# Kernel optimization log

Measured on AMD Instinct MI355X. Metric: run time of the kernel, lower is better.

## Reference

```python
import jax, jax.numpy as jnp
import numpy as np
import math

B, F, M, H, W, PD, KS = 2048, 512, 16, 32, 32, 64, 11
K = KS * KS
R = KS // 2
SIGMA = float(KS) / 3.0
HW = H * W


def _pos_encoding(gaze):
    # (B,2) -> (B,PD); interleaved sin/cos per axis
    half = PD // 2
    div = jnp.exp(jnp.arange(0, half, 2, dtype=jnp.float32) * -(math.log(10000.0) / half))  # (half/2,)
    def enc(p):  # p: (B,1)
        s = jnp.sin(p * div)
        c = jnp.cos(p * div)
        return jnp.stack([s, c], axis=-1).reshape(-1, half)
    return jnp.concatenate([enc(gaze[:, 0:1]), enc(gaze[:, 1:2])], axis=1)


def _adaptive_avg_pool3(x):
    # x: (B,C,H,W) -> (B,C,3,3), matching torch AdaptiveAvgPool2d(3)
    def bounds(n):
        return [(int(np.floor(i * n / 3)), int(np.ceil((i + 1) * n / 3))) for i in range(3)]
    hb, wb = bounds(x.shape[2]), bounds(x.shape[3])
    rows = []
    for (h0, h1) in hb:
        cols = [x[:, :, h0:h1, w0:w1].mean(axis=(2, 3)) for (w0, w1) in wb]
        rows.append(jnp.stack(cols, axis=-1))
    return jnp.stack(rows, axis=-2)  # (B,C,3,3)


def _conv(x, k, b):
    y = jax.lax.conv_general_dilated(x, k, (1, 1), 'SAME',
                                     dimension_numbers=('NCHW', 'OIHW', 'NCHW'))
    return y + b[None, :, None, None]


def setup_inputs() -> dict:
    key = jax.random.key(0)
    ks = jax.random.split(key, 20)
    n = lambda i, shp, sc=0.02: (jax.random.normal(ks[i], shp, dtype=jnp.float32) * sc)
    inp = {
        'features': jax.random.normal(ks[0], (B, F), dtype=jnp.float32),
        'cell_state': jax.random.normal(ks[1], (B, M, H, W), dtype=jnp.float32),
        'gaze_coords': jax.random.uniform(ks[2], (B, 2), dtype=jnp.float32),
        # input_gate: Linear(F+PD,256) -> ReLU -> Linear(256,128) -> ReLU
        'w1': n(3, (F + PD, 256)), 'b1': jnp.zeros((256,), jnp.float32),
        'w2': n(4, (256, 128)), 'b2': jnp.zeros((128,), jnp.float32),
        # write_value: Linear(128, M*K)
        'wv': n(5, (128, M * K)), 'bv': jnp.zeros((M * K,), jnp.float32),
        # strength_head: Linear(2M,64) -> ReLU -> Linear(64,1) -> Sigmoid
        'ws1': n(6, (2 * M, 64)), 'bs1': jnp.zeros((64,), jnp.float32),
        'ws2': n(7, (64, 1)), 'bs2': jnp.zeros((1,), jnp.float32),
        # output_gate convs + final linear
        'ck1': n(8, (128, M, 3, 3)), 'cb1': jnp.zeros((128,), jnp.float32),
        'ck2': n(9, (64, 128, 3, 3)), 'cb2': jnp.zeros((64,), jnp.float32),
        'wo': n(10, (64 * 9, 64 * 9)), 'bo': jnp.zeros((64 * 9,), jnp.float32),
    }
    return inp


def reference(features, cell_state, gaze_coords, w1, b1, w2, b2, wv, bv,
              ws1, bs1, ws2, bs2, ck1, cb1, ck2, cb2, wo, bo):
    # --- input gate + write values ---
    pe = _pos_encoding(gaze_coords)
    g = jax.nn.relu(jnp.concatenate([features, pe], axis=1) @ w1 + b1)
    g = jax.nn.relu(g @ w2 + b2)
    write_vals = (g @ wv + bv).reshape(B, K, M)

    # --- neighborhood geometry ---
    offs = jnp.arange(-R, R + 1)
    ox, oy = jnp.meshgrid(offs, offs, indexing='xy')
    ox, oy = ox.reshape(-1), oy.reshape(-1)  # (K,)
    gx = jnp.clip(gaze_coords[:, 0] * (W - 1), 0.0, W - 1.0)
    gy = jnp.clip(gaze_coords[:, 1] * (H - 1), 0.0, H - 1.0)
    x0 = jnp.floor(gx).astype(jnp.int32)
    y0 = jnp.floor(gy).astype(jnp.int32)
    xs = jnp.clip(x0[:, None] + ox[None, :], 0, W - 1)  # (B,K)
    ys = jnp.clip(y0[:, None] + oy[None, :], 0, H - 1)
    dx = xs.astype(jnp.float32) - gx[:, None]
    dy = ys.astype(jnp.float32) - gy[:, None]
    gauss = jnp.exp(-(dx * dx + dy * dy) / max(1e-6, 2.0 * SIGMA ** 2))
    nw = gauss / jnp.maximum(gauss.sum(axis=1, keepdims=True), 1e-8)  # (B,K)

    # --- gather previous values ---
    idx = ys * W + xs  # (B,K) flat indices
    cell_flat = cell_state.reshape(B, M, HW)
    prev = jnp.take_along_axis(cell_flat, idx[:, None, :], axis=2).transpose(0, 2, 1)  # (B,K,M)

    # --- learned per-cell strength gate ---
    gate_in = jnp.concatenate([prev, write_vals], axis=-1)  # (B,K,2M)
    s = jax.nn.relu(gate_in @ ws1 + bs1)
    gstr = jax.nn.sigmoid(s @ ws2 + bs2)  # (B,K,1)
    w_all = nw[:, :, None] * gstr  # (B,K,1)
    new_vals = (1.0 - w_all) * prev + w_all * write_vals  # (B,K,M)

    # --- weighted scatter-add with normalization ---
    b_idx = jnp.arange(B)[:, None]
    den = jnp.zeros((B, HW), jnp.float32).at[b_idx, idx].add(w_all[..., 0])
    num = jnp.zeros((B, HW, M), jnp.float32).at[b_idx, idx].add(w_all * new_vals)
    keep = 1.0 - jnp.minimum(den, 1.0)  # (B,HW)
    updated_flat = keep[:, None, :] * cell_flat + num.transpose(0, 2, 1)
    updated = updated_flat.reshape(B, M, H, W)

    # --- output gate ---
    y = jax.nn.relu(_conv(updated, ck1, cb1))
    y = jax.nn.relu(_conv(y, ck2, cb2))
    y = _adaptive_avg_pool3(y).reshape(B, -1)  # (B,576)
    out = y @ wo + bo
    return out, updated
```

## Files before the change

kernel.cpp:

```cpp
#include <hip/hip_runtime.h>
#include <hip/hip_bf16.h>
#include <math.h>

#define NB 2048
#define NF 512
#define NM 16
#define NK 121
#define NMK 1936

typedef __attribute__((ext_vector_type(8))) short bf16x8;
typedef __attribute__((ext_vector_type(4))) float f32x4;

#define MFMA __builtin_amdgcn_mfma_f32_16x16x32_bf16

static __device__ __forceinline__ unsigned short f2b(float f) {
  unsigned int u = __float_as_uint(f);
  unsigned int lsb = (u >> 16) & 1u;
  u += 0x7fffu + lsb;
  return (unsigned short)(u >> 16);
}

static __device__ __forceinline__ unsigned cvtpk(float lo, float hi) {
  unsigned r;
  asm("v_cvt_pk_bf16_f32 %0, %1, %2" : "=v"(r) : "v"(lo), "v"(hi));
  return r;
}

__global__ __launch_bounds__(256) void k_pack(
    const float* __restrict__ ck1, const float* __restrict__ ck2,
    unsigned short* __restrict__ ap1, unsigned short* __restrict__ ap2) {
  int i = blockIdx.x * 256 + threadIdx.x;
  if (i < 20480) {
    int j = i & 7, lane = (i >> 3) & 63;
    int m2 = (i >> 9) & 1, kc = (i >> 10) % 5, w = i / 5120;
    int c1 = w * 32 + m2 * 16 + (lane & 15);
    int k = kc * 32 + ((lane >> 4) << 3) + j;
    int s = k >> 4, ci = k & 15;
    float v = 0.f;
    if (s < 9) v = ck1[((c1 * 16 + ci) * 3 + s / 3) * 3 + (s % 3)];
    ap1[i] = f2b(v);
  }
  int i2 = i - 20480;
  if (i2 >= 0 && i2 < 73728) {
    int j = i2 & 7, lane = (i2 >> 3) & 63;
    int kc = (i2 >> 9) & 3, s = (i2 >> 11) % 9, mt = i2 / 18432;
    int c2 = mt * 16 + (lane & 15);
    int c1 = kc * 32 + ((lane >> 4) << 3) + j;
    float v = ck2[((c2 * 128 + c1) * 3 + s / 3) * 3 + (s % 3)];
    ap2[i2] = f2b(v);
  }
}

__global__ __launch_bounds__(256) void k_mlp(
    const float* __restrict__ feat, const float* __restrict__ gaze,
    const float* __restrict__ w1, const float* __restrict__ b1,
    const float* __restrict__ w2, const float* __restrict__ b2,
    const float* __restrict__ wv, const float* __restrict__ bv,
    float* __restrict__ wvout) {
  __shared__ float xs[4][576];
  __shared__ float g1[4][256];
  __shared__ float g2[4][128];
  const int t = threadIdx.x;
  const int b0 = blockIdx.x * 4;

  for (int e = t; e < 4 * 512; e += 256) {
    int r = e >> 9, i = e & 511;
    xs[r][i] = feat[(size_t)(b0 + r) * NF + i];
  }
  if (t < 4 * 64) {
    int r = t >> 6, i = t & 63;
    int axis = i >> 5;
    int ii = i & 31;
    int jj = ii >> 1;
    int isc = ii & 1;
    float p = gaze[(size_t)(b0 + r) * 2 + axis];
    float dv = expf(-(float)(2 * jj) * 0.28782313662425575f);
    float ang = p * dv;
    xs[r][512 + i] = isc ? cosf(ang) : sinf(ang);
  }
  __syncthreads();
  {
    float acc[4];
    float bb = b1[t];
#pragma unroll
    for (int r = 0; r < 4; r++) acc[r] = bb;
#pragma unroll 8
    for (int i = 0; i < 576; i++) {
      float w = w1[(size_t)i * 256 + t];
#pragma unroll
      for (int r = 0; r < 4; r++) acc[r] = fmaf(xs[r][i], w, acc[r]);
    }
#pragma unroll
    for (int r = 0; r < 4; r++) g1[r][t] = fmaxf(acc[r], 0.f);
  }
  __syncthreads();
  if (t < 128) {
    float acc[4];
    float bb = b2[t];
#pragma unroll
    for (int r = 0; r < 4; r++) acc[r] = bb;
#pragma unroll 8
    for (int i = 0; i < 256; i++) {
      float w = w2[(size_t)i * 128 + t];
#pragma unroll
      for (int r = 0; r < 4; r++) acc[r] = fmaf(g1[r][i], w, acc[r]);
    }
#pragma unroll
    for (int r = 0; r < 4; r++) g2[r][t] = fmaxf(acc[r], 0.f);
  }
  __syncthreads();
  {
    float acc7[7][4];
    float accT[4];
#pragma unroll
    for (int jj = 0; jj < 7; jj++) {
      float bb = bv[t + 256 * jj];
#pragma unroll
      for (int r = 0; r < 4; r++) acc7[jj][r] = bb;
    }
    {
      float bb = (t < 144) ? bv[1792 + t] : 0.f;
#pragma unroll
      for (int r = 0; r < 4; r++) accT[r] = bb;
    }
#pragma unroll 2
    for (int i = 0; i < 128; i++) {
      float g[4];
#pragma unroll
      for (int r = 0; r < 4; r++) g[r] = g2[r][i];
      const float* wrow = wv + (size_t)i * NMK;
#pragma unroll
      for (int jj = 0; jj < 7; jj++) {
        float w = wrow[t + 256 * jj];
#pragma unroll
        for (int r = 0; r < 4; r++) acc7[jj][r] = fmaf(g[r], w, acc7[jj][r]);
      }
      if (t < 144) {
        float w = wrow[1792 + t];
#pragma unroll
        for (int r = 0; r < 4; r++) accT[r] = fmaf(g[r], w, accT[r]);
      }
    }
#pragma unroll
    for (int r = 0; r < 4; r++) {
      float* orow = wvout + (size_t)(b0 + r) * NMK;
#pragma unroll
      for (int jj = 0; jj < 7; jj++) orow[t + 256 * jj] = acc7[jj][r];
      if (t < 144) orow[1792 + t] = accT[r];
    }
  }
}

__global__ __launch_bounds__(256) void k_update(
    const float* __restrict__ cell, const float* __restrict__ gaze,
    const float* __restrict__ wvin,
    const float* __restrict__ ws1, const float* __restrict__ bs1,
    const float* __restrict__ ws2, const float* __restrict__ bs2,
    float* __restrict__ updated, unsigned short* __restrict__ ubf) {
  __shared__ float numl[16][129];
  __shared__ float denl[128];
  __shared__ float ws1s[2048];
  __shared__ float bs1s[64];
  __shared__ float ws2s[64];
  __shared__ float nws[121];
  __shared__ float z2part[2][128];
  __shared__ float gsum_s;
  __shared__ float bs2s;
  const int t = threadIdx.x;
  const int b = blockIdx.x;
  const int kk = t & 127;
  const int hf = t >> 7;

  for (int e = t; e < 16 * 129; e += 256) ((float*)numl)[e] = 0.f;
  if (t < 128) denl[t] = 0.f;
  for (int e = t; e < 2048; e += 256) ws1s[e] = ws1[e];
  if (t < 64) { bs1s[t] = bs1[t]; ws2s[t] = ws2[t]; }
  if (t == 0) bs2s = bs2[0];

  const float gx = fminf(fmaxf(gaze[(size_t)b * 2 + 0] * 31.f, 0.f), 31.f);
  const float gy = fminf(fmaxf(gaze[(size_t)b * 2 + 1] * 31.f, 0.f), 31.f);
  const int x0 = (int)floorf(gx);
  const int y0 = (int)floorf(gy);
  const int wx0 = max(0, x0 - 5);
  const int wy0 = max(0, y0 - 5);

  int xi = 0, yi = 0;
  if (kk < NK) {
    int ox = kk % 11 - 5;
    int oy = kk / 11 - 5;
    xi = min(max(x0 + ox, 0), 31);
    yi = min(max(y0 + oy, 0), 31);
    if (hf == 0) {
      float dx = (float)xi - gx, dy = (float)yi - gy;
      nws[kk] = expf(-(dx * dx + dy * dy) * (9.0f / 242.0f));
    }
  }
  __syncthreads();
  if (t < 64) {
    float s = nws[t] + ((t + 64 < NK) ? nws[t + 64] : 0.f);
    s += __shfl_xor(s, 1, 64);
    s += __shfl_xor(s, 2, 64);
    s += __shfl_xor(s, 4, 64);
    s += __shfl_xor(s, 8, 64);
    s += __shfl_xor(s, 16, 64);
    s += __shfl_xor(s, 32, 64);
    if (t == 0) gsum_s = fmaxf(s, 1e-8f);
  }
  __syncthreads();

  float prev[16], wvv[16];
  if (kk < NK) {
    const int idx = yi * 32 + xi;
#pragma unroll
    for (int m = 0; m < 16; m++) prev[m] = cell[(size_t)b * 16384 + m * 1024 + idx];
#pragma unroll
    for (int m = 0; m < 16; m++) wvv[m] = wvin[(size_t)b * NMK + kk * 16 + m];
    float z2p = 0.f;
    const int j0 = hf * 32;
    for (int j = j0; j < j0 + 32; j++) {
      float z = bs1s[j];
#pragma unroll
      for (int i = 0; i < 16; i++) z = fmaf(prev[i], ws1s[i * 64 + j], z);
#pragma unroll
      for (int i = 0; i < 16; i++) z = fmaf(wvv[i], ws1s[(16 + i) * 64 + j], z);
      z = fmaxf(z, 0.f);
      z2p = fmaf(z, ws2s[j], z2p);
    }
    z2part[hf][kk] = z2p;
  }
  __syncthreads();

  if (t < NK) {
    const float nw = nws[t] / gsum_s;
    const int local = (yi - wy0) * 11 + (xi - wx0);
    float z2 = bs2s + z2part[0][t] + z2part[1][t];
    float gstr = 1.f / (1.f + expf(-z2));
    float w = nw * gstr;
    atomicAdd(&denl[local], w);
#pragma unroll
    for (int m = 0; m < 16; m++) {
      float nv = (1.f - w) * prev[m] + w * wvv[m];
      atomicAdd(&numl[m][local], w * nv);
    }
  }
  __syncthreads();

  for (int e = t; e < 16384; e += 256) {
    int m = e >> 10, hw = e & 1023;
    int yy = hw >> 5, xx = hw & 31;
    int wy = yy - wy0, wx = xx - wx0;
    float dv = 0.f, nm = 0.f;
    if ((unsigned)wy < 11u && (unsigned)wx < 11u) {
      int local = wy * 11 + wx;
      dv = denl[local];
      nm = numl[m][local];
    }
    float keep = 1.f - fminf(dv, 1.f);
    updated[(size_t)b * 16384 + e] = keep * cell[(size_t)b * 16384 + e] + nm;
  }

  unsigned* ub32 = (unsigned*)ubf + (size_t)b * 9248;
  for (int e = t; e < 8192; e += 256) {
    int p = e & 7;
    int hw = e >> 3;
    int yy = hw >> 5, xx = hw & 31;
    int wy = yy - wy0, wx = xx - wx0;
    float dv = 0.f, n0 = 0.f, n1 = 0.f;
    if ((unsigned)wy < 11u && (unsigned)wx < 11u) {
      int local = wy * 11 + wx;
      dv = denl[local];
      n0 = numl[2 * p][local];
      n1 = numl[2 * p + 1][local];
    }
    float keep = 1.f - fminf(dv, 1.f);
    float v0 = keep * cell[(size_t)b * 16384 + (2 * p) * 1024 + hw] + n0;
    float v1 = keep * cell[(size_t)b * 16384 + (2 * p + 1) * 1024 + hw] + n1;
    ub32[((yy + 1) * 34 + (xx + 1)) * 8 + p] = cvtpk(v0, v1);
  }
  for (int e = t; e < 1056; e += 256) {
    int j = e & 7, pos = e >> 3;
    int row, col;
    if (pos < 34)       { row = 0;             col = pos; }
    else if (pos < 68)  { row = 33;            col = pos - 34; }
    else if (pos < 100) { row = pos - 68 + 1;  col = 0; }
    else                { row = pos - 100 + 1; col = 33; }
    ub32[(row * 34 + col) * 8 + j] = 0u;
  }
}

__global__ __launch_bounds__(256, 2) void k_conv3(
    const unsigned short* __restrict__ ubf,
    const unsigned short* __restrict__ ap1, const float* __restrict__ cb1,
    const unsigned short* __restrict__ ap2, const float* __restrict__ cb2,
    float* __restrict__ ypool) {
  __shared__ unsigned short y1[6][34][136];
  const int t = threadIdx.x;
  const int b = blockIdx.x;
  const int lane = t & 63;
  const int w = t >> 6;
  const int ln = lane & 15;
  const int q = lane >> 4;
  const int qh = q >> 1, ql = q & 1;

  const unsigned short* ubb = ubf + (size_t)b * 18496;

  bf16x8 a2[9][4];
#pragma unroll
  for (int s = 0; s < 9; s++)
#pragma unroll
    for (int kc = 0; kc < 4; kc++)
      a2[s][kc] = *(const bf16x8*)(ap2 + (size_t)((w * 36 + s * 4 + kc) * 64 + lane) * 8);

  f32x4 cb2r;
  {
    int c2b = w * 16 + q * 4;
    cb2r = f32x4{cb2[c2b], cb2[c2b + 1], cb2[c2b + 2], cb2[c2b + 3]};
  }

  int po1[5];
#pragma unroll
  for (int kc = 0; kc < 5; kc++) {
    int s = 2 * kc + qh;
    if (s > 8) s = 0;
    po1[kc] = (s / 3) * 544 + (s % 3) * 16;
  }

  for (int e = t; e < 816; e += 256) {
    int w8 = e % 68;
    int r2 = e / 68;
    ((unsigned*)y1)[(r2 >> 1) * 2312 + ((r2 & 1) ? 2244 : 0) + w8] = 0u;
  }

  f32x4 PL0 = {0.f, 0.f, 0.f, 0.f}, PL1 = PL0, PL2 = PL0;
  f32x4 PH0 = PL0, PH1 = PL0, PH2 = PL0;

#pragma unroll 1
  for (int ti = 0; ti < 8; ti++) {
    const int r0 = ti * 4;

    bf16x8 a1[5][2];
#pragma unroll
    for (int kc = 0; kc < 5; kc++)
#pragma unroll
      for (int m2 = 0; m2 < 2; m2++)
        a1[kc][m2] = *(const bf16x8*)(ap1 + (size_t)(((w * 5 + kc) * 2 + m2) * 64 + lane) * 8);
    f32x4 cb1r[2];
#pragma unroll
    for (int m2 = 0; m2 < 2; m2++) {
      int c1b = w * 32 + m2 * 16 + q * 4;
      cb1r[m2] = f32x4{cb1[c1b], cb1[c1b + 1], cb1[c1b + 2], cb1[c1b + 3]};
    }

#pragma unroll 2
    for (int nt = 0; nt < 12; nt++) {
      const int ry = nt >> 1, h = nt & 1;
      const int gy1 = r0 - 1 + ry;
      const int gyc = min(max(gy1, 0), 31);
      const int x = h * 16 + ln;
      const unsigned short* bp = ubb + gyc * 544 + x * 16 + ql * 8;
      bf16x8 f0 = *(const bf16x8*)(bp + po1[0]);
      bf16x8 f1 = *(const bf16x8*)(bp + po1[1]);
      bf16x8 f2 = *(const bf16x8*)(bp + po1[2]);
      bf16x8 f3 = *(const bf16x8*)(bp + po1[3]);
      bf16x8 f4 = *(const bf16x8*)(bp + po1[4]);
      f32x4 acc0 = cb1r[0], acc1 = cb1r[1];
      acc0 = MFMA(a1[0][0], f0, acc0, 0, 0, 0); acc1 = MFMA(a1[0][1], f0, acc1, 0, 0, 0);
      acc0 = MFMA(a1[1][0], f1, acc0, 0, 0, 0); acc1 = MFMA(a1[1][1], f1, acc1, 0, 0, 0);
      acc0 = MFMA(a1[2][0], f2, acc0, 0, 0, 0); acc1 = MFMA(a1[2][1], f2, acc1, 0, 0, 0);
      acc0 = MFMA(a1[3][0], f3, acc0, 0, 0, 0); acc1 = MFMA(a1[3][1], f3, acc1, 0, 0, 0);
      acc0 = MFMA(a1[4][0], f4, acc0, 0, 0, 0); acc1 = MFMA(a1[4][1], f4, acc1, 0, 0, 0);
      const bool inr = ((unsigned)gy1 < 32u);
#pragma unroll
      for (int m2 = 0; m2 < 2; m2++) {
        f32x4 a = m2 ? acc1 : acc0;
        float v0 = inr ? fmaxf(a[0], 0.f) : 0.f;
        float v1 = inr ? fmaxf(a[1], 0.f) : 0.f;
        float v2 = inr ? fmaxf(a[2], 0.f) : 0.f;
        float v3 = inr ? fmaxf(a[3], 0.f) : 0.f;
        uint2 pk;
        pk.x = cvtpk(v0, v1);
        pk.y = cvtpk(v2, v3);
        *(uint2*)&y1[ry][1 + x][w * 32 + m2 * 16 + q * 4] = pk;
      }
    }
    __syncthreads();

#pragma unroll
    for (int h = 0; h < 2; h++) {
      const int xg = h * 16 + ln;
      const unsigned short* yb = &y1[0][xg][q * 8];
      f32x4 A0 = cb2r, A1 = cb2r, A2 = cb2r, A3 = cb2r;
#pragma unroll
      for (int yr = 0; yr < 6; yr++)
#pragma unroll
        for (int kc = 0; kc < 4; kc++)
#pragma unroll
          for (int dx = 0; dx < 3; dx++) {
            bf16x8 fr = *(const bf16x8*)(yb + yr * 4624 + dx * 136 + kc * 32);
#pragma unroll
            for (int dy = 0; dy < 3; dy++) {
              const int rr = yr - dy;
              if (rr < 0 || rr > 3) continue;
              f32x4& ac = (rr == 0) ? A0 : ((rr == 1) ? A1 : ((rr == 2) ? A2 : A3));
              ac = MFMA(a2[dy * 3 + dx][kc], fr, ac, 0, 0, 0);
            }
          }
#pragma unroll
      for (int rr = 0; rr < 4; rr++) {
        const int grow = r0 + rr;
        const float rm0 = (grow <= 10) ? 1.f : 0.f;
        const float rm1 = (grow >= 10 && grow <= 21) ? 1.f : 0.f;
        const float rm2 = (grow >= 21) ? 1.f : 0.f;
        f32x4 v = (rr == 0) ? A0 : ((rr == 1) ? A1 : ((rr == 2) ? A2 : A3));
        v[0] = fmaxf(v[0], 0.f);
        v[1] = fmaxf(v[1], 0.f);
        v[2] = fmaxf(v[2], 0.f);
        v[3] = fmaxf(v[3], 0.f);
        if (h == 0) {
          PL0 += v * rm0; PL1 += v * rm1; PL2 += v * rm2;
        } else {
          PH0 += v * rm0; PH1 += v * rm1; PH2 += v * rm2;
        }
      }
    }
    __syncthreads();
  }

  const float mA0 = (ln <= 10) ? 1.f : 0.f;
  const float mA1 = (ln >= 10) ? 1.f : 0.f;
  const float mB1 = (ln <= 5) ? 1.f : 0.f;
  const float mB2 = (ln >= 5) ? 1.f : 0.f;
  f32x4 t00 = PL0 * mA0, t01 = PL0 * mA1 + PH0 * mB1, t02 = PH0 * mB2;
  f32x4 t10 = PL1 * mA0, t11 = PL1 * mA1 + PH1 * mB1, t12 = PH1 * mB2;
  f32x4 t20 = PL2 * mA0, t21 = PL2 * mA1 + PH2 * mB1, t22 = PH2 * mB2;

  {
    f32x4* tv[9] = {&t00, &t01, &t02, &t10, &t11, &t12, &t20, &t21, &t22};
#pragma unroll
    for (int i = 0; i < 9; i++) {
      f32x4& v = *tv[i];
#pragma unroll
      for (int c = 0; c < 4; c++) {
        float s = v[c];
        s += __shfl_xor(s, 1, 64);
        s += __shfl_xor(s, 2, 64);
        s += __shfl_xor(s, 4, 64);
        s += __shfl_xor(s, 8, 64);
        v[c] = s;
      }
    }
  }

  float* yp = ypool + (size_t)b * 576 + (w * 16 + q * 4) * 9;
#define PWRITE(tv, ph, pw)                                                      \
  if (ln == (ph * 3 + pw)) {                                                    \
    const float dv = 1.f / (float)(((ph == 1) ? 12 : 11) * ((pw == 1) ? 12 : 11)); \
    yp[0 * 9 + ph * 3 + pw] = tv[0] * dv;                                       \
    yp[1 * 9 + ph * 3 + pw] = tv[1] * dv;                                       \
    yp[2 * 9 + ph * 3 + pw] = tv[2] * dv;                                       \
    yp[3 * 9 + ph * 3 + pw] = tv[3] * dv;                                       \
  }
  PWRITE(t00, 0, 0) PWRITE(t01, 0, 1) PWRITE(t02, 0, 2)
  PWRITE(t10, 1, 0) PWRITE(t11, 1, 1) PWRITE(t12, 1, 2)
  PWRITE(t20, 2, 0) PWRITE(t21, 2, 1) PWRITE(t22, 2, 2)
#undef PWRITE
}

__global__ __launch_bounds__(256) void k_out(
    const float* __restrict__ ypool, const float* __restrict__ wo,
    const float* __restrict__ bo, float* __restrict__ out) {
  __shared__ float ys[8][576];
  const int t = threadIdx.x;
  const int b0 = blockIdx.x * 8;
  for (int e = t; e < 8 * 576; e += 256) {
    int r = e / 576, i = e % 576;
    ys[r][i] = ypool[(size_t)(b0 + r) * 576 + i];
  }
  __syncthreads();
  for (int j = t; j < 576; j += 256) {
    float acc[8];
    float bb = bo[j];
#pragma unroll
    for (int r = 0; r < 8; r++) acc[r] = bb;
#pragma unroll 4
    for (int i = 0; i < 576; i++) {
      float w = wo[(size_t)i * 576 + j];
#pragma unroll
      for (int r = 0; r < 8; r++) acc[r] = fmaf(ys[r][i], w, acc[r]);
    }
#pragma unroll
    for (int r = 0; r < 8; r++) out[(size_t)(b0 + r) * 576 + j] = acc[r];
  }
}

extern "C" void kernel_launch(void* const* d_in, const int* in_sizes, int n_in,
                              void* d_out, int out_size, void* d_ws, size_t ws_size,
                              hipStream_t stream) {
  (void)in_sizes; (void)n_in; (void)out_size;
  const float* feat = (const float*)d_in[0];
  const float* cell = (const float*)d_in[1];
  const float* gaze = (const float*)d_in[2];
  const float* w1   = (const float*)d_in[3];
  const float* b1   = (const float*)d_in[4];
  const float* w2   = (const float*)d_in[5];
  const float* b2   = (const float*)d_in[6];
  const float* wv   = (const float*)d_in[7];
  const float* bv   = (const float*)d_in[8];
  const float* ws1  = (const float*)d_in[9];
  const float* bs1  = (const float*)d_in[10];
  const float* ws2  = (const float*)d_in[11];
  const float* bs2  = (const float*)d_in[12];
  const float* ck1  = (const float*)d_in[13];
  const float* cb1  = (const float*)d_in[14];
  const float* ck2  = (const float*)d_in[15];
  const float* cb2  = (const float*)d_in[16];
  const float* wo   = (const float*)d_in[17];
  const float* bo   = (const float*)d_in[18];

  float* out0    = (float*)d_out;
  float* updated = out0 + (size_t)NB * 576;
  float* wvout   = (float*)d_ws;
  float* ypool   = wvout + (size_t)NB * NMK;
  unsigned short* ap1 = (unsigned short*)(ypool + (size_t)NB * 576);
  unsigned short* ap2 = ap1 + 20480;
  unsigned short* ubf = ap2 + 73728;

  const size_t fixed_bytes = ((size_t)NB * (NMK + 576)) * 4 + (size_t)94208 * 2;
  const size_t wsz = ws_size ? ws_size : ((size_t)1 << 30);
  int chunk = 2048;
  while (chunk > 128 && fixed_bytes + (size_t)chunk * 36992 > wsz) chunk >>= 1;

  k_pack<<<dim3(368), dim3(256), 0, stream>>>(ck1, ck2, ap1, ap2);
  k_mlp<<<dim3(NB / 4), dim3(256), 0, stream>>>(feat, gaze, w1, b1, w2, b2, wv, bv, wvout);
  for (int b0 = 0; b0 < NB; b0 += chunk) {
    const int n = (NB - b0 < chunk) ? (NB - b0) : chunk;
    k_update<<<dim3(n), dim3(256), 0, stream>>>(
        cell + (size_t)b0 * 16384, gaze + (size_t)b0 * 2,
        wvout + (size_t)b0 * NMK, ws1, bs1, ws2, bs2,
        updated + (size_t)b0 * 16384, ubf);
    k_conv3<<<dim3(n), dim3(256), 0, stream>>>(
        ubf, ap1, cb1, ap2, cb2, ypool + (size_t)b0 * 576);
  }
  k_out<<<dim3(NB / 8), dim3(256), 0, stream>>>(ypool, wo, bo, out0);
}
```

Before: 1.093 ms.

## Use ring buffer for conv1 rows, raise occupancy, restructure output GEMV

The conv3 kernel now keeps a 6-slot ring buffer of conv1 output rows, so each tile after the first computes only 4 new rows instead of recomputing 6 including the halo rows. The shared buffer drops the padding column (the right-edge read wraps to a zero column), and launch bounds ask for 3 blocks per SM. The output linear kernel handles 4 batch rows per block with twice as many blocks and fixed per-thread column assignments. The ring buffer relies on the zeroed halo slots and the wrap indexing staying correct, and the higher occupancy target may force register spills given the large a2 register array.

```diff
diff --git a/kernel.cpp b/kernel.cpp
--- a/kernel.cpp
+++ b/kernel.cpp
@@ -288,12 +288,13 @@
   }
 }
 
-__global__ __launch_bounds__(256, 2) void k_conv3(
+#define Y1ROW 4488
+__global__ __launch_bounds__(256, 3) void k_conv3(
     const unsigned short* __restrict__ ubf,
     const unsigned short* __restrict__ ap1, const float* __restrict__ cb1,
     const unsigned short* __restrict__ ap2, const float* __restrict__ cb2,
     float* __restrict__ ypool) {
-  __shared__ unsigned short y1[6][34][136];
+  __shared__ unsigned short y1[6][33][136];
   const int t = threadIdx.x;
   const int b = blockIdx.x;
   const int lane = t & 63;
@@ -325,10 +326,9 @@
     po1[kc] = (s / 3) * 544 + (s % 3) * 16;
   }
 
-  for (int e = t; e < 816; e += 256) {
-    int w8 = e % 68;
-    int r2 = e / 68;
-    ((unsigned*)y1)[(r2 >> 1) * 2312 + ((r2 & 1) ? 2244 : 0) + w8] = 0u;
+  for (int e = t; e < 6 * 68; e += 256) {
+    int s = e / 68, wd = e % 68;
+    ((unsigned*)y1)[s * (Y1ROW / 2) + wd] = 0u;
   }
 
   f32x4 PL0 = {0.f, 0.f, 0.f, 0.f}, PL1 = PL0, PL2 = PL0;
@@ -351,10 +351,13 @@
       cb1r[m2] = f32x4{cb1[c1b], cb1[c1b + 1], cb1[c1b + 2], cb1[c1b + 3]};
     }
 
+    const int nrow = (ti == 0) ? 6 : 4;
+    const int abase = (ti == 0) ? -1 : r0 + 1;
 #pragma unroll 2
-    for (int nt = 0; nt < 12; nt++) {
+    for (int nt = 0; nt < nrow * 2; nt++) {
       const int ry = nt >> 1, h = nt & 1;
-      const int gy1 = r0 - 1 + ry;
+      const int gy1 = abase + ry;
+      const int slot = (gy1 + 1) % 6;
       const int gyc = min(max(gy1, 0), 31);
       const int x = h * 16 + ln;
       const unsigned short* bp = ubb + gyc * 544 + x * 16 + ql * 8;
@@ -380,15 +383,34 @@
         uint2 pk;
         pk.x = cvtpk(v0, v1);
         pk.y = cvtpk(v2, v3);
-        *(uint2*)&y1[ry][1 + x][w * 32 + m2 * 16 + q * 4] = pk;
+        *(uint2*)&y1[slot][1 + x][w * 32 + m2 * 16 + q * 4] = pk;
       }
     }
     __syncthreads();
 
+    int rowoff[6];
+    {
+      int s0 = (r0) % 6;
+#pragma unroll
+      for (int yr = 0; yr < 6; yr++) {
+        int s = s0 + yr;
+        if (s >= 6) s -= 6;
+        rowoff[yr] = s * Y1ROW;
+      }
+    }
 #pragma unroll
     for (int h = 0; h < 2; h++) {
       const int xg = h * 16 + ln;
-      const unsigned short* yb = &y1[0][xg][q * 8];
+      const unsigned short* rp[6];
+#pragma unroll
+      for (int yr = 0; yr < 6; yr++) rp[yr] = &y1[0][0][0] + rowoff[yr] + q * 8;
+      int pco[3];
+#pragma unroll
+      for (int dx = 0; dx < 3; dx++) {
+        int pc = xg + dx;
+        if (pc == 33) pc = 0;
+        pco[dx] = pc * 136;
+      }
       f32x4 A0 = cb2r, A1 = cb2r, A2 = cb2r, A3 = cb2r;
 #pragma unroll
       for (int yr = 0; yr < 6; yr++)
@@ -396,7 +418,7 @@
         for (int kc = 0; kc < 4; kc++)
 #pragma unroll
           for (int dx = 0; dx < 3; dx++) {
-            bf16x8 fr = *(const bf16x8*)(yb + yr * 4624 + dx * 136 + kc * 32);
+            bf16x8 fr = *(const bf16x8*)(rp[yr] + pco[dx] + kc * 32);
 #pragma unroll
             for (int dy = 0; dy < 3; dy++) {
               const int rr = yr - dy;
@@ -469,27 +491,45 @@
 __global__ __launch_bounds__(256) void k_out(
     const float* __restrict__ ypool, const float* __restrict__ wo,
     const float* __restrict__ bo, float* __restrict__ out) {
-  __shared__ float ys[8][576];
+  __shared__ float ys[4][576];
   const int t = threadIdx.x;
-  const int b0 = blockIdx.x * 8;
-  for (int e = t; e < 8 * 576; e += 256) {
+  const int b0 = blockIdx.x * 4;
+  for (int e = t; e < 4 * 576; e += 256) {
     int r = e / 576, i = e % 576;
     ys[r][i] = ypool[(size_t)(b0 + r) * 576 + i];
   }
   __syncthreads();
-  for (int j = t; j < 576; j += 256) {
-    float acc[8];
-    float bb = bo[j];
-#pragma unroll
-    for (int r = 0; r < 8; r++) acc[r] = bb;
-#pragma unroll 4
-    for (int i = 0; i < 576; i++) {
-      float w = wo[(size_t)i * 576 + j];
-#pragma unroll
-      for (int r = 0; r < 8; r++) acc[r] = fmaf(ys[r][i], w, acc[r]);
-    }
-#pragma unroll
-    for (int r = 0; r < 8; r++) out[(size_t)(b0 + r) * 576 + j] = acc[r];
+  float a0[4], a1[4], aT[4];
+  {
+    float bb0 = bo[t], bb1 = bo[t + 256];
+    float bbT = (t < 64) ? bo[512 + t] : 0.f;
+#pragma unroll
+    for (int r = 0; r < 4; r++) { a0[r] = bb0; a1[r] = bb1; aT[r] = bbT; }
+  }
+#pragma unroll 2
+  for (int i = 0; i < 576; i++) {
+    const float* wr = wo + (size_t)i * 576;
+    float w0 = wr[t], w1 = wr[t + 256];
+    float g[4];
+#pragma unroll
+    for (int r = 0; r < 4; r++) g[r] = ys[r][i];
+#pragma unroll
+    for (int r = 0; r < 4; r++) {
+      a0[r] = fmaf(g[r], w0, a0[r]);
+      a1[r] = fmaf(g[r], w1, a1[r]);
+    }
+    if (t < 64) {
+      float wT = wr[512 + t];
+#pragma unroll
+      for (int r = 0; r < 4; r++) aT[r] = fmaf(g[r], wT, aT[r]);
+    }
+  }
+#pragma unroll
+  for (int r = 0; r < 4; r++) {
+    float* orow = out + (size_t)(b0 + r) * 576;
+    orow[t] = a0[r];
+    orow[t + 256] = a1[r];
+    if (t < 64) orow[512 + t] = aT[r];
   }
 }
 
@@ -541,5 +581,5 @@
     k_conv3<<<dim3(n), dim3(256), 0, stream>>>(
         ubf, ap1, cb1, ap2, cb2, ypool + (size_t)b0 * 576);
   }
-  k_out<<<dim3(NB / 8), dim3(256), 0, stream>>>(ypool, wo, bo, out0);
-}
+  k_out<<<dim3(NB / 8 * 2), dim3(256), 0, stream>>>(ypool, wo, bo, out0);
+}
```

Measured after the change: 2.272 ms. +107.8%, slower.
